# Performance work log

Hardware: AMD Instinct MI355X
Metric: run time of the kernel (lower is better)

Reference implementation:

```python
import jax, jax.numpy as jnp
import numpy as np
import math

TAU_PLUS = 20.0
TAU_MINUS = 20.0
A_PLUS = 0.01
A_MINUS = 0.01
W_MAX = 1.0
W_MIN = 0.0
TARGET_RATE = 0.1
HOMEO = 0.001
RATE_ALPHA = 0.01
DT = 1.0


def setup_inputs() -> dict:
    key = jax.random.key(0)
    k1, k2, k3, k4 = jax.random.split(key, 4)
    B, PRE, POST = 1024, 4096, 4096
    return {
        "pre_spikes": jax.random.uniform(k1, (B, PRE), dtype=jnp.float32),
        "post_spikes": jax.random.uniform(k2, (B, POST), dtype=jnp.float32),
        "weights": jax.random.uniform(k3, (POST, PRE), dtype=jnp.float32) * 0.5,
        "pre_trace": jnp.zeros((B, PRE), dtype=jnp.float32),
        "post_trace": jnp.zeros((B, POST), dtype=jnp.float32),
        "running_rate": jax.random.uniform(k4, (POST,), dtype=jnp.float32) * 0.2,
    }


def reference(pre_spikes, post_spikes, weights, pre_trace, post_trace, running_rate):
    B = pre_spikes.shape[0]
    # trace decay
    pre_tr = pre_trace * math.exp(-DT / TAU_PLUS)
    post_tr = post_trace * math.exp(-DT / TAU_MINUS)
    # STDP weight update (learn=True, auto_scale=False)
    dw_plus = A_PLUS * jnp.einsum('bp,bq->pq', post_spikes, pre_tr) / B
    dw_minus = -A_MINUS * jnp.einsum('bp,bq->pq', post_tr, pre_spikes) / B
    dw_homeo = -HOMEO * (running_rate - TARGET_RATE)[:, None]
    new_weights = jnp.clip(weights + dw_plus + dw_minus + dw_homeo, W_MIN, W_MAX)
    # homeostatic rate EMA
    batch_rate = post_spikes.mean(axis=0)
    new_rate = running_rate * (1.0 - RATE_ALPHA) + RATE_ALPHA * batch_rate
    # trace update
    new_pre_trace = pre_tr + pre_spikes
    new_post_trace = post_tr + post_spikes
    # postsynaptic current with updated weights
    current = pre_spikes @ new_weights.T  # (B, POST)
    return current, new_weights, new_pre_trace, new_post_trace, new_rate
```

## Files before the change

kernel.cpp:

```cpp
#include <hip/hip_runtime.h>
#include <hip/hip_fp8.h>

typedef __attribute__((ext_vector_type(8))) short short8;
typedef __attribute__((ext_vector_type(4))) float floatx4;
typedef __attribute__((ext_vector_type(8))) int int8v;
typedef __attribute__((ext_vector_type(4))) int int4v;

#define LDS_PTR(x) ((__attribute__((address_space(3))) unsigned int*)(x))
#define GLB_PTR(x) ((const __attribute__((address_space(1))) unsigned int*)(x))

__device__ __forceinline__ unsigned short f2bf(float f) {
    unsigned int u = __float_as_uint(f);
    unsigned int r = (u + 0x7FFFu + ((u >> 16) & 1u)) >> 16;
    return (unsigned short)r;
}
__device__ __forceinline__ unsigned char f2fp8(float f) {
    __hip_fp8_e4m3 v(f);
    return (unsigned char)v.__x;
}
__device__ __forceinline__ float fp82f(unsigned int u) {
    __hip_fp8_e4m3 v;
    v.__x = (__hip_fp8_storage_t)(u & 0xFF);
    return (float)v;
}

__global__ __launch_bounds__(256) void prep_post_kernel(
    const float* __restrict__ S, const float* __restrict__ T,
    float* __restrict__ traceOut, unsigned char* __restrict__ At,
    int C, int K2, int Bsz, float dp)
{
    __shared__ float sT[64][65];
    __shared__ float tT[64][65];
    const int t = threadIdx.x;
    const int r0 = blockIdx.y * 64, c0 = blockIdx.x * 64;
#pragma unroll
    for (int i = 0; i < 4; ++i) {
        int rl = (t >> 4) + i * 16;
        int cl = (t & 15) * 4;
        size_t g = (size_t)(r0 + rl) * C + c0 + cl;
        float4 s4 = *(const float4*)&S[g];
        float4 t4 = *(const float4*)&T[g];
        float4 o;
        o.x = fmaf(t4.x, dp, s4.x); o.y = fmaf(t4.y, dp, s4.y);
        o.z = fmaf(t4.z, dp, s4.z); o.w = fmaf(t4.w, dp, s4.w);
        *(float4*)&traceOut[g] = o;
        sT[rl][cl + 0] = s4.x; sT[rl][cl + 1] = s4.y;
        sT[rl][cl + 2] = s4.z; sT[rl][cl + 3] = s4.w;
        tT[rl][cl + 0] = t4.x; tT[rl][cl + 1] = t4.y;
        tT[rl][cl + 2] = t4.z; tT[rl][cl + 3] = t4.w;
    }
    __syncthreads();
#pragma unroll
    for (int i = 0; i < 4; ++i) {
        int cl = (t >> 4) + i * 16;
        int rl = (t & 15) * 4;
        uchar4 a, b;
        a.x = f2fp8(sT[rl + 0][cl]); a.y = f2fp8(sT[rl + 1][cl]);
        a.z = f2fp8(sT[rl + 2][cl]); a.w = f2fp8(sT[rl + 3][cl]);
        b.x = f2fp8(tT[rl + 0][cl]); b.y = f2fp8(tT[rl + 1][cl]);
        b.z = f2fp8(tT[rl + 2][cl]); b.w = f2fp8(tT[rl + 3][cl]);
        *(uchar4*)&At[(size_t)(c0 + cl) * K2 + r0 + rl] = a;
        *(uchar4*)&At[(size_t)(c0 + cl) * K2 + Bsz + r0 + rl] = b;
    }
}

__global__ __launch_bounds__(256) void prep_pre_kernel(
    const float* __restrict__ S, const float* __restrict__ T,
    float* __restrict__ traceOut, unsigned char* __restrict__ Bt,
    unsigned short* __restrict__ preBf,
    int C, int K2, int Bsz, float dp)
{
    __shared__ float sT[64][65];
    __shared__ float tT[64][65];
    const int t = threadIdx.x;
    const int r0 = blockIdx.y * 64, c0 = blockIdx.x * 64;
#pragma unroll
    for (int i = 0; i < 4; ++i) {
        int rl = (t >> 4) + i * 16;
        int cl = (t & 15) * 4;
        size_t g = (size_t)(r0 + rl) * C + c0 + cl;
        float4 s4 = *(const float4*)&S[g];
        float4 t4 = *(const float4*)&T[g];
        float4 o;
        o.x = fmaf(t4.x, dp, s4.x); o.y = fmaf(t4.y, dp, s4.y);
        o.z = fmaf(t4.z, dp, s4.z); o.w = fmaf(t4.w, dp, s4.w);
        *(float4*)&traceOut[g] = o;
        ushort4 pb = { f2bf(s4.x), f2bf(s4.y), f2bf(s4.z), f2bf(s4.w) };
        *(ushort4*)&preBf[g] = pb;
        sT[rl][cl + 0] = s4.x; sT[rl][cl + 1] = s4.y;
        sT[rl][cl + 2] = s4.z; sT[rl][cl + 3] = s4.w;
        tT[rl][cl + 0] = t4.x; tT[rl][cl + 1] = t4.y;
        tT[rl][cl + 2] = t4.z; tT[rl][cl + 3] = t4.w;
    }
    __syncthreads();
#pragma unroll
    for (int i = 0; i < 4; ++i) {
        int cl = (t >> 4) + i * 16;
        int rl = (t & 15) * 4;
        uchar4 a, b;
        a.x = f2fp8(tT[rl + 0][cl]); a.y = f2fp8(tT[rl + 1][cl]);
        a.z = f2fp8(tT[rl + 2][cl]); a.w = f2fp8(tT[rl + 3][cl]);
        b.x = f2fp8(-sT[rl + 0][cl]); b.y = f2fp8(-sT[rl + 1][cl]);
        b.z = f2fp8(-sT[rl + 2][cl]); b.w = f2fp8(-sT[rl + 3][cl]);
        *(uchar4*)&Bt[(size_t)(c0 + cl) * K2 + r0 + rl] = a;
        *(uchar4*)&Bt[(size_t)(c0 + cl) * K2 + Bsz + r0 + rl] = b;
    }
}

__global__ __launch_bounds__(256) void rate_kernel(
    const unsigned char* __restrict__ At, const float* __restrict__ rr,
    float* __restrict__ new_rate, int K2, int Bsz)
{
    const int w = threadIdx.x >> 6, l = threadIdx.x & 63;
    const int p = blockIdx.x * 4 + w;
    const unsigned char* row = At + (size_t)p * K2;
    float s = 0.f;
    for (int k = l * 16; k < Bsz; k += 1024) {
        int4v v = *(const int4v*)&row[k];
#pragma unroll
        for (int wd = 0; wd < 4; ++wd) {
            unsigned int u = (unsigned int)v[wd];
            s += fp82f(u) + fp82f(u >> 8) + fp82f(u >> 16) + fp82f(u >> 24);
        }
    }
#pragma unroll
    for (int off = 32; off > 0; off >>= 1) s += __shfl_xor(s, off, 64);
    if (l == 0)
        new_rate[p] = rr[p] * 0.99f + 0.01f * (s / (float)Bsz);
}

__global__ __launch_bounds__(256) void dw_fp8_kernel(
    const unsigned char* __restrict__ A, const unsigned char* __restrict__ B,
    int K, int N, float s,
    const float* __restrict__ Wold, const float* __restrict__ rr,
    float* __restrict__ outF, unsigned short* __restrict__ outBf)
{
    constexpr int BM = 128, BN = 128, BK = 128;
    __shared__ unsigned char smem[65536];

    const int t = threadIdx.x;
    const int l = t & 63;
    const int w = t >> 6;
    const int wm = w >> 1, wn = w & 1;
    const int bm = blockIdx.y, bn = blockIdx.x;

    floatx4 acc[4][4] = {};

    auto stage = [&](int buf, int k0) {
        unsigned char* la = smem + buf * 16384;
        unsigned char* lb = smem + 32768 + buf * 16384;
#pragma unroll
        for (int i = 0; i < 4; ++i) {
            int ci = i * 256 + t;
            int r = ci >> 3, sc = ci & 7;
            int g = sc ^ (r & 7);
            const unsigned char* gpA = A + (size_t)(bm * BM + r) * K + k0 + g * 16;
            __builtin_amdgcn_global_load_lds(GLB_PTR(gpA),
                LDS_PTR(la + ci * 16), 16, 0, 0);
            const unsigned char* gpB = B + (size_t)(bn * BN + r) * K + k0 + g * 16;
            __builtin_amdgcn_global_load_lds(GLB_PTR(gpB),
                LDS_PTR(lb + ci * 16), 16, 0, 0);
        }
    };

    stage(0, 0);
    __syncthreads();

    const int nT = K / BK;
    int cur = 0;
    for (int tt = 0; tt < nT; ++tt) {
        if (tt + 1 < nT) stage(cur ^ 1, (tt + 1) * BK);

        const unsigned char* la = smem + cur * 16384;
        const unsigned char* lb = smem + 32768 + cur * 16384;
        const int c = l >> 4;
        const int m = l & 15;
        int8v af[4], bf[4];
#pragma unroll
        for (int i = 0; i < 4; ++i) {
            int ra = wm * 64 + i * 16 + m;
            int s0 = (2 * c) ^ (ra & 7), s1 = (2 * c + 1) ^ (ra & 7);
            int4v lo = *(const int4v*)&la[ra * BK + s0 * 16];
            int4v hi = *(const int4v*)&la[ra * BK + s1 * 16];
            af[i][0] = lo[0]; af[i][1] = lo[1]; af[i][2] = lo[2]; af[i][3] = lo[3];
            af[i][4] = hi[0]; af[i][5] = hi[1]; af[i][6] = hi[2]; af[i][7] = hi[3];
        }
#pragma unroll
        for (int j = 0; j < 4; ++j) {
            int rb = wn * 64 + j * 16 + m;
            int s0 = (2 * c) ^ (rb & 7), s1 = (2 * c + 1) ^ (rb & 7);
            int4v lo = *(const int4v*)&lb[rb * BK + s0 * 16];
            int4v hi = *(const int4v*)&lb[rb * BK + s1 * 16];
            bf[j][0] = lo[0]; bf[j][1] = lo[1]; bf[j][2] = lo[2]; bf[j][3] = lo[3];
            bf[j][4] = hi[0]; bf[j][5] = hi[1]; bf[j][6] = hi[2]; bf[j][7] = hi[3];
        }
#pragma unroll
        for (int i = 0; i < 4; ++i)
#pragma unroll
            for (int j = 0; j < 4; ++j)
                acc[i][j] = __builtin_amdgcn_mfma_scale_f32_16x16x128_f8f6f4(
                    af[i], bf[j], acc[i][j], 0, 0, 0, 0x7f, 0, 0x7f);

        asm volatile("s_waitcnt vmcnt(0)" ::: "memory");
        __builtin_amdgcn_s_barrier();
        cur ^= 1;
    }

    __syncthreads();
    float* sOut = (float*)smem;
#pragma unroll
    for (int i = 0; i < 4; ++i)
#pragma unroll
        for (int r = 0; r < 4; ++r) {
            const int row = wm * 64 + i * 16 + (l >> 4) * 4 + r;
#pragma unroll
            for (int j = 0; j < 4; ++j) {
                const int col = wn * 64 + j * 16 + (l & 15);
                sOut[row * 128 + col] = acc[i][j][r];
            }
        }
    __syncthreads();

    const int pBase = bm * BM;
    const int qBase = bn * BN;
#pragma unroll
    for (int k = 0; k < 16; ++k) {
        const int ci = k * 256 + t;
        const int row = ci >> 5;
        const int cc = (ci & 31) * 4;
        const int p = pBase + row;
        const int q = qBase + cc;
        const size_t idx = (size_t)p * N + q;
        float4 a4 = *(const float4*)&sOut[ci * 4];
        float4 w4 = *(const float4*)&Wold[idx];
        const float hp = -0.001f * (rr[p] - 0.1f);
        float4 v;
        v.x = fminf(fmaxf(fmaf(s, a4.x, w4.x + hp), 0.f), 1.f);
        v.y = fminf(fmaxf(fmaf(s, a4.y, w4.y + hp), 0.f), 1.f);
        v.z = fminf(fmaxf(fmaf(s, a4.z, w4.z + hp), 0.f), 1.f);
        v.w = fminf(fmaxf(fmaf(s, a4.w, w4.w + hp), 0.f), 1.f);
        *(float4*)&outF[idx] = v;
        ushort4 b4 = { f2bf(v.x), f2bf(v.y), f2bf(v.z), f2bf(v.w) };
        *(ushort4*)&outBf[idx] = b4;
    }
}

__global__ __launch_bounds__(256) void mfma_gemm_bt(
    const unsigned short* __restrict__ A,
    const unsigned short* __restrict__ Bm,
    int K, int N, float* __restrict__ outF)
{
    constexpr int BM = 128, BN = 128, BK = 64;
    __shared__ unsigned char smem[65536];

    const int t = threadIdx.x;
    const int l = t & 63;
    const int w = t >> 6;
    const int wm = w >> 1, wn = w & 1;
    const int bm = blockIdx.y, bn = blockIdx.x;

    floatx4 acc[4][4] = {};

    auto stage = [&](int buf, int k0) {
        unsigned short* la = (unsigned short*)(smem + buf * 16384);
        unsigned short* lb = (unsigned short*)(smem + 32768 + buf * 16384);
#pragma unroll
        for (int i = 0; i < 4; ++i) {
            int ci = i * 256 + t;
            int r = ci >> 3, sc = ci & 7;
            int g = sc ^ (r & 7);
            const unsigned short* gpA = A + (size_t)(bm * BM + r) * K + k0 + g * 8;
            __builtin_amdgcn_global_load_lds(GLB_PTR(gpA),
                LDS_PTR(la + ci * 8), 16, 0, 0);
            const unsigned short* gpB = Bm + (size_t)(bn * BN + r) * K + k0 + g * 8;
            __builtin_amdgcn_global_load_lds(GLB_PTR(gpB),
                LDS_PTR(lb + ci * 8), 16, 0, 0);
        }
    };

    stage(0, 0);
    __syncthreads();

    const int nT = K / BK;
    int cur = 0;
    for (int tt = 0; tt < nT; ++tt) {
        if (tt + 1 < nT) stage(cur ^ 1, (tt + 1) * BK);

        const unsigned short* la = (const unsigned short*)(smem + cur * 16384);
        const unsigned short* lb = (const unsigned short*)(smem + 32768 + cur * 16384);
        const int q = l >> 4;
        const int m = l & 15;
        short8 af[4][2], bf[4][2];
#pragma unroll
        for (int i = 0; i < 4; ++i) {
            int ra = wm * 64 + i * 16 + m;
#pragma unroll
            for (int ks = 0; ks < 2; ++ks) {
                int c2 = ks * 4 + q;
                af[i][ks] = *(const short8*)&la[ra * BK + ((c2 ^ (ra & 7)) * 8)];
            }
        }
#pragma unroll
        for (int j = 0; j < 4; ++j) {
            int rb = wn * 64 + j * 16 + m;
#pragma unroll
            for (int ks = 0; ks < 2; ++ks) {
                int c2 = ks * 4 + q;
                bf[j][ks] = *(const short8*)&lb[rb * BK + ((c2 ^ (rb & 7)) * 8)];
            }
        }
#pragma unroll
        for (int ks = 0; ks < 2; ++ks)
#pragma unroll
            for (int i = 0; i < 4; ++i)
#pragma unroll
                for (int j = 0; j < 4; ++j)
                    acc[i][j] = __builtin_amdgcn_mfma_f32_16x16x32_bf16(
                        af[i][ks], bf[j][ks], acc[i][j], 0, 0, 0);

        asm volatile("s_waitcnt vmcnt(0)" ::: "memory");
        __builtin_amdgcn_s_barrier();
        cur ^= 1;
    }

    __syncthreads();
    float* sOut = (float*)smem;
#pragma unroll
    for (int i = 0; i < 4; ++i)
#pragma unroll
        for (int r = 0; r < 4; ++r) {
            const int row = wm * 64 + i * 16 + (l >> 4) * 4 + r;
#pragma unroll
            for (int j = 0; j < 4; ++j) {
                const int col = wn * 64 + j * 16 + (l & 15);
                sOut[row * 128 + col] = acc[i][j][r];
            }
        }
    __syncthreads();

    const int pBase = bm * BM;
    const int qBase = bn * BN;
#pragma unroll
    for (int k = 0; k < 16; ++k) {
        const int ci = k * 256 + t;
        const int row = ci >> 5;
        const int cc = (ci & 31) * 4;
        float4 v = *(const float4*)&sOut[ci * 4];
        *(float4*)&outF[(size_t)(pBase + row) * N + qBase + cc] = v;
    }
}

extern "C" void kernel_launch(void* const* d_in, const int* in_sizes, int n_in,
                              void* d_out, int out_size, void* d_ws, size_t ws_size,
                              hipStream_t stream)
{
    const float* pre_spikes   = (const float*)d_in[0];
    const float* post_spikes  = (const float*)d_in[1];
    const float* weights      = (const float*)d_in[2];
    const float* pre_trace    = (const float*)d_in[3];
    const float* post_trace   = (const float*)d_in[4];
    const float* running_rate = (const float*)d_in[5];

    const int POST = in_sizes[5];
    const int PRE  = in_sizes[2] / POST;
    const int Bsz  = in_sizes[0] / PRE;
    const int K2   = 2 * Bsz;

    const size_t nCur   = (size_t)Bsz * POST;
    const size_t nW     = (size_t)POST * PRE;
    const size_t nPreT  = (size_t)Bsz * PRE;
    const size_t nPostT = (size_t)Bsz * POST;

    float* out_current    = (float*)d_out;
    float* out_weights    = out_current + nCur;
    float* out_pre_trace  = out_weights + nW;
    float* out_post_trace = out_pre_trace + nPreT;
    float* out_rate       = out_post_trace + nPostT;

    unsigned char* At     = (unsigned char*)d_ws;
    unsigned char* Bt     = At + (size_t)POST * K2;
    unsigned short* preBf = (unsigned short*)(Bt + (size_t)PRE * K2);
    unsigned short* wBf   = preBf + nPreT;

    const float dp = 0.95122942450071400910f;
    const float s  = dp * (0.01f / (float)Bsz);

    prep_post_kernel<<<dim3(POST / 64, Bsz / 64), 256, 0, stream>>>(
        post_spikes, post_trace, out_post_trace, At, POST, K2, Bsz, dp);
    prep_pre_kernel<<<dim3(PRE / 64, Bsz / 64), 256, 0, stream>>>(
        pre_spikes, pre_trace, out_pre_trace, Bt, preBf, PRE, K2, Bsz, dp);

    rate_kernel<<<POST / 4, 256, 0, stream>>>(
        At, running_rate, out_rate, K2, Bsz);

    dw_fp8_kernel<<<dim3(PRE / 128, POST / 128), 256, 0, stream>>>(
        At, Bt, K2, PRE, s, weights, running_rate, out_weights, wBf);

    mfma_gemm_bt<<<dim3(POST / 128, Bsz / 128), 256, 0, stream>>>(
        preBf, wBf, PRE, POST, out_current);
}
```

Baseline: 309.3 us.

## Prefetch old weights before dW GEMM loop and halve current-GEMM M tile

In the dW kernel, the old weight tile and homeostatic offsets are loaded into registers before the K loop, so their global latency overlaps with the MFMA main loop instead of stalling the epilogue. The current GEMM moves from 128x128 to 64x128 tiles, doubling the grid from 256 to 512 blocks so the CUs are better covered for the 1024x4096 output. The trade-offs are 64+ extra live registers in the dW kernel, which may cut occupancy, and more B-operand reloads across M tiles in the second GEMM.

Measured after the change: 324.3 us. +4.9%, slower.

```diff
diff --git a/kernel.cpp b/kernel.cpp
--- a/kernel.cpp
+++ b/kernel.cpp
@@ -164,6 +164,20 @@
     };
 
     stage(0, 0);
+
+    const int pBase = bm * BM;
+    const int qBase = bn * BN;
+    float4 wold[16];
+    float hp[16];
+#pragma unroll
+    for (int k = 0; k < 16; ++k) {
+        const int ci = k * 256 + t;
+        const int row = ci >> 5;
+        const int cc = (ci & 31) * 4;
+        wold[k] = *(const float4*)&Wold[(size_t)(pBase + row) * N + qBase + cc];
+        hp[k] = -0.001f * (rr[pBase + row] - 0.1f);
+    }
+
     __syncthreads();
 
     const int nT = K / BK;
@@ -221,24 +235,18 @@
         }
     __syncthreads();
 
-    const int pBase = bm * BM;
-    const int qBase = bn * BN;
 #pragma unroll
     for (int k = 0; k < 16; ++k) {
         const int ci = k * 256 + t;
         const int row = ci >> 5;
         const int cc = (ci & 31) * 4;
-        const int p = pBase + row;
-        const int q = qBase + cc;
-        const size_t idx = (size_t)p * N + q;
+        const size_t idx = (size_t)(pBase + row) * N + qBase + cc;
         float4 a4 = *(const float4*)&sOut[ci * 4];
-        float4 w4 = *(const float4*)&Wold[idx];
-        const float hp = -0.001f * (rr[p] - 0.1f);
         float4 v;
-        v.x = fminf(fmaxf(fmaf(s, a4.x, w4.x + hp), 0.f), 1.f);
-        v.y = fminf(fmaxf(fmaf(s, a4.y, w4.y + hp), 0.f), 1.f);
-        v.z = fminf(fmaxf(fmaf(s, a4.z, w4.z + hp), 0.f), 1.f);
-        v.w = fminf(fmaxf(fmaf(s, a4.w, w4.w + hp), 0.f), 1.f);
+        v.x = fminf(fmaxf(fmaf(s, a4.x, wold[k].x + hp[k]), 0.f), 1.f);
+        v.y = fminf(fmaxf(fmaf(s, a4.y, wold[k].y + hp[k]), 0.f), 1.f);
+        v.z = fminf(fmaxf(fmaf(s, a4.z, wold[k].z + hp[k]), 0.f), 1.f);
+        v.w = fminf(fmaxf(fmaf(s, a4.w, wold[k].w + hp[k]), 0.f), 1.f);
         *(float4*)&outF[idx] = v;
         ushort4 b4 = { f2bf(v.x), f2bf(v.y), f2bf(v.z), f2bf(v.w) };
         *(ushort4*)&outBf[idx] = b4;
@@ -250,8 +258,8 @@
     const unsigned short* __restrict__ Bm,
     int K, int N, float* __restrict__ outF)
 {
-    constexpr int BM = 128, BN = 128, BK = 64;
-    __shared__ unsigned char smem[65536];
+    constexpr int BM = 64, BN = 128, BK = 64;
+    __shared__ unsigned char smem[49152];
 
     const int t = threadIdx.x;
     const int l = t & 63;
@@ -259,21 +267,29 @@
     const int wm = w >> 1, wn = w & 1;
     const int bm = blockIdx.y, bn = blockIdx.x;
 
-    floatx4 acc[4][4] = {};
+    floatx4 acc[2][4] = {};
 
     auto stage = [&](int buf, int k0) {
-        unsigned short* la = (unsigned short*)(smem + buf * 16384);
-        unsigned short* lb = (unsigned short*)(smem + 32768 + buf * 16384);
+        unsigned short* la = (unsigned short*)(smem + buf * 24576);
+        unsigned short* lb = (unsigned short*)(smem + buf * 24576 + 8192);
+#pragma unroll
+        for (int i = 0; i < 2; ++i) {
+            int ci = i * 256 + t;
+            int r = ci >> 3, sc = ci & 7;
+            int g = sc ^ (r & 7);
+            const unsigned short* gp =
+                A + (size_t)(bm * BM + r) * K + k0 + g * 8;
+            __builtin_amdgcn_global_load_lds(GLB_PTR(gp),
+                LDS_PTR(la + ci * 8), 16, 0, 0);
+        }
 #pragma unroll
         for (int i = 0; i < 4; ++i) {
             int ci = i * 256 + t;
             int r = ci >> 3, sc = ci & 7;
             int g = sc ^ (r & 7);
-            const unsigned short* gpA = A + (size_t)(bm * BM + r) * K + k0 + g * 8;
-            __builtin_amdgcn_global_load_lds(GLB_PTR(gpA),
-                LDS_PTR(la + ci * 8), 16, 0, 0);
-            const unsigned short* gpB = Bm + (size_t)(bn * BN + r) * K + k0 + g * 8;
-            __builtin_amdgcn_global_load_lds(GLB_PTR(gpB),
+            const unsigned short* gp =
+                Bm + (size_t)(bn * BN + r) * K + k0 + g * 8;
+            __builtin_amdgcn_global_load_lds(GLB_PTR(gp),
                 LDS_PTR(lb + ci * 8), 16, 0, 0);
         }
     };
@@ -286,14 +302,14 @@
     for (int tt = 0; tt < nT; ++tt) {
         if (tt + 1 < nT) stage(cur ^ 1, (tt + 1) * BK);
 
-        const unsigned short* la = (const unsigned short*)(smem + cur * 16384);
-        const unsigned short* lb = (const unsigned short*)(smem + 32768 + cur * 16384);
+        const unsigned short* la = (const unsigned short*)(smem + cur * 24576);
+        const unsigned short* lb = (const unsigned short*)(smem + cur * 24576 + 8192);
         const int q = l >> 4;
         const int m = l & 15;
-        short8 af[4][2], bf[4][2];
-#pragma unroll
-        for (int i = 0; i < 4; ++i) {
-            int ra = wm * 64 + i * 16 + m;
+        short8 af[2][2], bf[4][2];
+#pragma unroll
+        for (int i = 0; i < 2; ++i) {
+            int ra = wm * 32 + i * 16 + m;
 #pragma unroll
             for (int ks = 0; ks < 2; ++ks) {
                 int c2 = ks * 4 + q;
@@ -312,7 +328,7 @@
 #pragma unroll
         for (int ks = 0; ks < 2; ++ks)
 #pragma unroll
-            for (int i = 0; i < 4; ++i)
+            for (int i = 0; i < 2; ++i)
 #pragma unroll
                 for (int j = 0; j < 4; ++j)
                     acc[i][j] = __builtin_amdgcn_mfma_f32_16x16x32_bf16(
@@ -326,10 +342,10 @@
     __syncthreads();
     float* sOut = (float*)smem;
 #pragma unroll
-    for (int i = 0; i < 4; ++i)
+    for (int i = 0; i < 2; ++i)
 #pragma unroll
         for (int r = 0; r < 4; ++r) {
-            const int row = wm * 64 + i * 16 + (l >> 4) * 4 + r;
+            const int row = wm * 32 + i * 16 + (l >> 4) * 4 + r;
 #pragma unroll
             for (int j = 0; j < 4; ++j) {
                 const int col = wn * 64 + j * 16 + (l & 15);
@@ -341,7 +357,7 @@
     const int pBase = bm * BM;
     const int qBase = bn * BN;
 #pragma unroll
-    for (int k = 0; k < 16; ++k) {
+    for (int k = 0; k < 8; ++k) {
         const int ci = k * 256 + t;
         const int row = ci >> 5;
         const int cc = (ci & 31) * 4;
@@ -396,6 +412,6 @@
     dw_fp8_kernel<<<dim3(PRE / 128, POST / 128), 256, 0, stream>>>(
         At, Bt, K2, PRE, s, weights, running_rate, out_weights, wBf);
 
-    mfma_gemm_bt<<<dim3(POST / 128, Bsz / 128), 256, 0, stream>>>(
+    mfma_gemm_bt<<<dim3(POST / 128, Bsz / 64), 256, 0, stream>>>(
         preBf, wBf, PRE, POST, out_current);
 }
```
